# Kernel tuning notes

Hardware: AMD Instinct MI355X
Metric: run time of the kernel (lower is better)

The kernel has to match this reference:

```python
import jax, jax.numpy as jnp
import numpy as np

B, T, H, W, C = 8, 16, 128, 128, 3
PATCH = 8
MODEL_DIM = 512
FFN_DIM = 2048
NUM_BLOCKS = 4
NUM_HEADS = 8
LATENT_DIM = 64
NUM_LATENTS = 4096
ACTION_DIM = 16
PATCH_TOKEN_DIM = C * PATCH * PATCH  # 192


def setup_inputs() -> dict:
    key = jax.random.key(0)
    ks = jax.random.split(key, 12)
    g = lambda k, s: jax.random.normal(k, s, dtype=jnp.float32) * 0.02
    D, L = MODEL_DIM, NUM_BLOCKS
    return dict(
        videos=jax.random.uniform(ks[0], (B, T, H, W, C), dtype=jnp.float32),
        patch_w=g(ks[1], (PATCH_TOKEN_DIM, D)),
        patch_b=jnp.zeros((D,), jnp.float32),
        action_token=g(ks[2], (PATCH_TOKEN_DIM,)),
        ln1_g=jnp.ones((L, D), jnp.float32), ln1_b=jnp.zeros((L, D), jnp.float32),
        wqkv_s=g(ks[3], (L, D, 3 * D)), wo_s=g(ks[4], (L, D, D)),
        ln2_g=jnp.ones((L, D), jnp.float32), ln2_b=jnp.zeros((L, D), jnp.float32),
        wqkv_t=g(ks[5], (L, D, 3 * D)), wo_t=g(ks[6], (L, D, D)),
        ln3_g=jnp.ones((L, D), jnp.float32), ln3_b=jnp.zeros((L, D), jnp.float32),
        mlp_w1=g(ks[7], (L, D, FFN_DIM)), mlp_b1=jnp.zeros((L, FFN_DIM), jnp.float32),
        mlp_w2=g(ks[8], (L, FFN_DIM, D)), mlp_b2=jnp.zeros((L, D), jnp.float32),
        lnf_g=jnp.ones((D,), jnp.float32), lnf_b=jnp.zeros((D,), jnp.float32),
        out_w=g(ks[9], (D, LATENT_DIM)),
        codebook=g(ks[10], (NUM_LATENTS, LATENT_DIM)),
        action_w=g(ks[11], (LATENT_DIM, ACTION_DIM)),
    )


def _ln(x, g, b):
    m = jnp.mean(x, -1, keepdims=True)
    v = jnp.var(x, -1, keepdims=True)
    return (x - m) * jax.lax.rsqrt(v + 1e-5) * g + b


def _mha(x, wqkv, wo, causal):
    bsz, S, D = x.shape
    hd = D // NUM_HEADS
    q, k, v = jnp.split(x @ wqkv, 3, axis=-1)
    split = lambda t: t.reshape(bsz, S, NUM_HEADS, hd).transpose(0, 2, 1, 3)
    q, k, v = split(q), split(k), split(v)
    scores = jnp.einsum('bhqd,bhkd->bhqk', q, k) * (1.0 / np.sqrt(hd))
    if causal:
        mask = jnp.tril(jnp.ones((S, S), dtype=bool))
        scores = jnp.where(mask, scores, jnp.finfo(scores.dtype).min)
    o = jnp.einsum('bhqk,bhkd->bhqd', jax.nn.softmax(scores, axis=-1), v)
    return o.transpose(0, 2, 1, 3).reshape(bsz, S, D) @ wo


def _forward(videos, patch_w, patch_b, action_token, ln1_g, ln1_b, wqkv_s, wo_s,
             ln2_g, ln2_b, wqkv_t, wo_t, ln3_g, ln3_b, mlp_w1, mlp_b1, mlp_w2,
             mlp_b2, lnf_g, lnf_b, out_w, codebook, action_w):
    b, t = videos.shape[:2]
    hp, wp = H // PATCH, W // PATCH
    # patchify: (B,T,H,W,C) -> (B,T,N,p*p*C)
    x = videos.reshape(b, t, hp, PATCH, wp, PATCH, C)
    x = x.transpose(0, 1, 2, 4, 3, 5, 6).reshape(b, t, hp * wp, PATCH_TOKEN_DIM)
    # prepend learned action token per frame
    act = jnp.broadcast_to(action_token, (b, t, 1, PATCH_TOKEN_DIM))
    x = jnp.concatenate([act, x], axis=2)             # (B,T,S,Ep)
    S = x.shape[2]
    tok = x @ patch_w + patch_b                        # (B,T,S,D)
    for i in range(NUM_BLOCKS):
        # spatial attention within each frame
        h = _ln(tok, ln1_g[i], ln1_b[i]).reshape(b * t, S, MODEL_DIM)
        tok = tok + _mha(h, wqkv_s[i], wo_s[i], causal=False).reshape(b, t, S, MODEL_DIM)
        # temporal causal attention per spatial position
        h = _ln(tok, ln2_g[i], ln2_b[i]).transpose(0, 2, 1, 3).reshape(b * S, t, MODEL_DIM)
        h = _mha(h, wqkv_t[i], wo_t[i], causal=True)
        tok = tok + h.reshape(b, S, t, MODEL_DIM).transpose(0, 2, 1, 3)
        # MLP
        h = _ln(tok, ln3_g[i], ln3_b[i])
        tok = tok + jax.nn.gelu(h @ mlp_w1[i] + mlp_b1[i]) @ mlp_w2[i] + mlp_b2[i]
    tok = _ln(tok, lnf_g, lnf_b)
    # latent action per transition: action token of frames 1..T-1
    z = tok[:, 1:, 0, :] @ out_w                       # (B, T-1, latent_dim)
    # VQ: nearest-neighbor codebook lookup (squared-L2 argmin + gather)
    d = (jnp.sum(z * z, -1, keepdims=True)
         - 2.0 * (z @ codebook.T)
         + jnp.sum(codebook * codebook, -1))           # (B, T-1, num_latents)
    idx = jnp.argmin(d, axis=-1)                       # (B, T-1)
    z_q = codebook[idx]
    z_q = z + jax.lax.stop_gradient(z_q - z)           # straight-through
    latent_actions = jax.lax.stop_gradient(z_q)
    return latent_actions @ action_w                   # (B, T-1, action_dim)


def reference(videos, patch_w, patch_b, action_token, ln1_g, ln1_b, wqkv_s, wo_s,
              ln2_g, ln2_b, wqkv_t, wo_t, ln3_g, ln3_b, mlp_w1, mlp_b1, mlp_w2,
              mlp_b2, lnf_g, lnf_b, out_w, codebook, action_w):
    return _forward(videos, patch_w, patch_b, action_token, ln1_g, ln1_b, wqkv_s,
                    wo_s, ln2_g, ln2_b, wqkv_t, wo_t, ln3_g, ln3_b, mlp_w1,
                    mlp_b1, mlp_w2, mlp_b2, lnf_g, lnf_b, out_w, codebook, action_w)
```

## Files before the change

kernel.cpp:

```cpp
#include <hip/hip_runtime.h>
#include <hip/hip_bf16.h>

#define B_ 8
#define T_ 16
#define S_ 257
#define D_ 512
#define FFN_ 2048
#define NH_ 8
#define HD_ 64
#define PTD_ 192
#define NTOK (B_*T_*S_)
#define CH 4112
#define PCH 8224
#define WSCALE 64.0f
#define WINV 0.015625f

typedef unsigned int uint;
typedef unsigned short ushort;
typedef __attribute__((ext_vector_type(8))) _Float16 half8;
typedef __attribute__((ext_vector_type(4))) float f32x4;

__device__ __forceinline__ float warp_rsum(float v){
#pragma unroll
  for (int m = 32; m >= 1; m >>= 1) v += __shfl_xor(v, m);
  return v;
}
__device__ __forceinline__ float gelu_f(float x){
  float x3 = x*x*x;
  return 0.5f*x*(1.0f + tanhf(0.7978845608028654f*(x + 0.044715f*x3)));
}
__device__ __forceinline__ void split_f16(float f, ushort& h, ushort& l){
  _Float16 hh = (_Float16)f;
  float hf = (float)hh;
  _Float16 ll = (_Float16)(f - hf);
  h = __builtin_bit_cast(ushort, hh);
  l = __builtin_bit_cast(ushort, ll);
}
__device__ __forceinline__ ushort to_f16u(float f){
  return __builtin_bit_cast(ushort, (_Float16)f);
}
__device__ __forceinline__ float from_f16u(ushort u){
  return (float)__builtin_bit_cast(_Float16, u);
}
__device__ __forceinline__ void gload16(const ushort* g, ushort* l){
  __builtin_amdgcn_global_load_lds(
      (const __attribute__((address_space(1))) void*)(g),
      (__attribute__((address_space(3))) void*)(l),
      16, 0, 0);
}

__global__ __launch_bounds__(256) void ln_single(
    const float* __restrict__ x, const float* __restrict__ g,
    const float* __restrict__ bb, ushort* __restrict__ aH)
{
  int row = blockIdx.x * 4 + (threadIdx.x >> 6);
  int lane = threadIdx.x & 63;
  const float* xr = x + (long)row * D_;
  float4 u0 = *(const float4*)(xr + lane * 8);
  float4 u1 = *(const float4*)(xr + lane * 8 + 4);
  float s = u0.x + u0.y + u0.z + u0.w + u1.x + u1.y + u1.z + u1.w;
  s = warp_rsum(s);
  float mean = s * (1.0f / 512.0f);
  float d[8] = {u0.x - mean, u0.y - mean, u0.z - mean, u0.w - mean,
                u1.x - mean, u1.y - mean, u1.z - mean, u1.w - mean};
  float ss = 0.f;
#pragma unroll
  for (int i = 0; i < 8; i++) ss = fmaf(d[i], d[i], ss);
  ss = warp_rsum(ss);
  float rstd = rsqrtf(ss * (1.0f / 512.0f) + 1e-5f);
  int c = lane * 8;
  float4 g0 = *(const float4*)(g + c), g1 = *(const float4*)(g + c + 4);
  float4 b0 = *(const float4*)(bb + c), b1 = *(const float4*)(bb + c + 4);
  float y[8] = {d[0]*rstd*g0.x + b0.x, d[1]*rstd*g0.y + b0.y,
                d[2]*rstd*g0.z + b0.z, d[3]*rstd*g0.w + b0.w,
                d[4]*rstd*g1.x + b1.x, d[5]*rstd*g1.y + b1.y,
                d[6]*rstd*g1.z + b1.z, d[7]*rstd*g1.w + b1.w};
  ushort h[8];
#pragma unroll
  for (int i = 0; i < 8; i++) h[i] = to_f16u(y[i]);
  uint4 hv = make_uint4((uint)h[0] | ((uint)h[1] << 16), (uint)h[2] | ((uint)h[3] << 16),
                        (uint)h[4] | ((uint)h[5] << 16), (uint)h[6] | ((uint)h[7] << 16));
  *(uint4*)(aH + (long)row * 512 + c) = hv;
}

__global__ __launch_bounds__(256) void convert_w(
    const float* __restrict__ W, ushort* __restrict__ Whi, ushort* __restrict__ Wlo,
    int N, int K)
{
  __shared__ float Tt[64][65];
  const int tid = threadIdx.x;
  const int k0 = blockIdx.x << 6, n0 = blockIdx.y << 6;
  {
    int kk = tid >> 2, nb = (tid & 3) << 4;
#pragma unroll
    for (int q = 0; q < 4; q++) {
      float4 v = *(const float4*)(W + (long)(k0 + kk) * N + n0 + nb + 4 * q);
      Tt[kk][nb + 4*q + 0] = v.x; Tt[kk][nb + 4*q + 1] = v.y;
      Tt[kk][nb + 4*q + 2] = v.z; Tt[kk][nb + 4*q + 3] = v.w;
    }
  }
  __syncthreads();
  {
    int nn = tid >> 2, kb = (tid & 3) << 4;
    uint hw[8], lw[8];
#pragma unroll
    for (int q = 0; q < 8; q++) {
      float a = Tt[kb + 2*q][nn] * WSCALE, b = Tt[kb + 2*q + 1][nn] * WSCALE;
      ushort ha, la, hb, lb;
      split_f16(a, ha, la); split_f16(b, hb, lb);
      hw[q] = (uint)ha | ((uint)hb << 16); lw[q] = (uint)la | ((uint)lb << 16);
    }
    ushort* dh = Whi + (long)(n0 + nn) * K + k0 + kb;
    ushort* dl = Wlo + (long)(n0 + nn) * K + k0 + kb;
    ((uint4*)dh)[0] = make_uint4(hw[0], hw[1], hw[2], hw[3]);
    ((uint4*)dh)[1] = make_uint4(hw[4], hw[5], hw[6], hw[7]);
    ((uint4*)dl)[0] = make_uint4(lw[0], lw[1], lw[2], lw[3]);
    ((uint4*)dl)[1] = make_uint4(lw[4], lw[5], lw[6], lw[7]);
  }
}

template<int BM, int BN, int TM, int TN, int AMODE, bool ASPLIT, bool BSPLIT, bool BIAS, bool GELU, bool RESID, int SOUT>
__global__ __launch_bounds__(256) void gemm_mfma(
    const ushort* __restrict__ aHp, const ushort* __restrict__ aLp, int lda,
    const ushort* __restrict__ wtH, const ushort* __restrict__ wtL, int ldb,
    const float* __restrict__ bias, float* __restrict__ C,
    ushort* __restrict__ coH, ushort* __restrict__ vOut,
    const float* __restrict__ videos, const float* __restrict__ atok,
    int M, int N, int K)
{
  constexpr int NWC = BN / (TN * 16);
  constexpr int NBUF = (AMODE == 0) ? 2 : 1;
  __shared__ __align__(16) ushort sAh[NBUF * BM * 32];
  __shared__ __align__(16) ushort sAl[(AMODE == 1) ? 128 * 32 : 8];
  __shared__ __align__(16) ushort sBh[NBUF * BN * 32];
  __shared__ __align__(16) ushort sBl[BSPLIT ? NBUF * BN * 32 : 8];
  const int tid = threadIdx.x;
  int m0, n0;
  if (AMODE == 0) {
    const int gx = gridDim.x, gy = gridDim.y;
    const int nwg = gx * gy;
    const int o = blockIdx.y * gx + blockIdx.x;
    const int q = nwg >> 3, r = nwg & 7;
    const int xcd = o & 7, idx = o >> 3;
    const int wgid = (xcd < r ? xcd * (q + 1) : r * (q + 1) + (xcd - r) * q) + idx;
    const int mi = wgid / gy, ni = wgid - mi * gy;
    m0 = mi * BM; n0 = ni * BN;
  } else {
    m0 = blockIdx.x * BM; n0 = blockIdx.y * BN;
  }
  const int wid = tid >> 6, lane = tid & 63;
  const int lrow = lane & 15, lkg = lane >> 4;
  const int wr = wid / NWC, wc = wid % NWC;
  const int wrb = wr * TM * 16, wcb = wc * TN * 16;
  f32x4 acc[TM][TN];
#pragma unroll
  for (int mi = 0; mi < TM; mi++)
#pragma unroll
    for (int ni = 0; ni < TN; ni++) acc[mi][ni] = (f32x4){0.f, 0.f, 0.f, 0.f};

  if (AMODE == 0) {
    auto stage = [&](int k0, int d) {
      {
        int row = tid >> 2, cp = tid & 3;
        int csrc = cp ^ ((row >> 1) & 3);
        int ar = m0 + row; if (ar > M - 1) ar = M - 1;
        gload16(aHp + (long)ar * lda + k0 + csrc * 8, &sAh[d * (BM * 32) + tid * 8]);
      }
      if constexpr (BM == 128) {
        int chunk = tid + 256;
        int row = chunk >> 2, cp = chunk & 3;
        int csrc = cp ^ ((row >> 1) & 3);
        int ar = m0 + row; if (ar > M - 1) ar = M - 1;
        gload16(aHp + (long)ar * lda + k0 + csrc * 8, &sAh[d * (BM * 32) + chunk * 8]);
      }
      if (BN == 128) {
#pragma unroll
        for (int i = 0; i < 2; i++) {
          int chunk = tid + 256 * i;
          int row = chunk >> 2, cp = chunk & 3;
          int csrc = cp ^ ((row >> 1) & 3);
          gload16(wtH + (long)(n0 + row) * ldb + k0 + csrc * 8, &sBh[d * 4096 + chunk * 8]);
        }
      } else {
        int chunk = tid;
        int row = chunk >> 2, cp = chunk & 3;
        int csrc = cp ^ ((row >> 1) & 3);
        gload16(wtH + (long)(n0 + row) * ldb + k0 + csrc * 8, &sBh[d * 2048 + chunk * 8]);
        if (BSPLIT)
          gload16(wtL + (long)(n0 + row) * ldb + k0 + csrc * 8, &sBl[d * 2048 + chunk * 8]);
      }
    };
    const int nt = K >> 5;
    stage(0, 0);
    if (nt > 1) stage(32, 1);
    constexpr int LPS = ((BM == 128) ? 2 : 1) + ((BN == 128) ? 2 : (BSPLIT ? 2 : 1));
    for (int t = 0; t < nt; t++) {
      const int cur = t & 1;
      if (t + 1 < nt) {
        if constexpr (LPS == 4) {
          asm volatile("s_waitcnt vmcnt(4)" ::: "memory");
        } else if constexpr (LPS == 3) {
          asm volatile("s_waitcnt vmcnt(3)" ::: "memory");
        } else {
          asm volatile("s_waitcnt vmcnt(2)" ::: "memory");
        }
      } else {
        asm volatile("s_waitcnt vmcnt(0)" ::: "memory");
      }
      __builtin_amdgcn_s_barrier();
      const int aBase = cur * (BM * 32);
      const int bBase = cur * ((BN == 128) ? 4096 : 2048);
      half8 aHf[TM], bHf[TN], bLf[BSPLIT ? TN : 1];
#pragma unroll
      for (int mi = 0; mi < TM; mi++) {
        int ar = wrb + mi * 16 + lrow;
        int ac = (ar * 4 + (lkg ^ ((ar >> 1) & 3))) * 8;
        aHf[mi] = *(const half8*)&sAh[aBase + ac];
      }
#pragma unroll
      for (int ni = 0; ni < TN; ni++) {
        int br = wcb + ni * 16 + lrow;
        int bc = (br * 4 + (lkg ^ ((br >> 1) & 3))) * 8;
        bHf[ni] = *(const half8*)&sBh[bBase + bc];
        if (BSPLIT) bLf[ni] = *(const half8*)&sBl[bBase + bc];
      }
      asm volatile("s_waitcnt lgkmcnt(0)" ::: "memory");
      __builtin_amdgcn_sched_barrier(0);
      __builtin_amdgcn_s_barrier();
      if (t + 2 < nt) stage((t + 2) << 5, cur);
      __builtin_amdgcn_s_setprio(1);
#pragma unroll
      for (int ni = 0; ni < TN; ni++) {
        if (BSPLIT) {
#pragma unroll
          for (int mi = 0; mi < TM; mi++)
            acc[mi][ni] = __builtin_amdgcn_mfma_f32_16x16x32_f16(aHf[mi], bLf[ni], acc[mi][ni], 0, 0, 0);
        }
#pragma unroll
        for (int mi = 0; mi < TM; mi++)
          acc[mi][ni] = __builtin_amdgcn_mfma_f32_16x16x32_f16(aHf[mi], bHf[ni], acc[mi][ni], 0, 0, 0);
      }
      __builtin_amdgcn_s_setprio(0);
      __builtin_amdgcn_sched_barrier(0);
    }
  } else {
    const int rowa = tid >> 1, kba = (tid & 1) << 4;
    const int cb0 = (tid & 1) * 2;
    const int swa = (rowa >> 1) & 3;
    int bt_p = 0, s_p = 0;
    { int ar = m0 + rowa; bt_p = ar / 257; s_p = ar - bt_p * 257; }
    for (int k0 = 0; k0 < K; k0 += 32) {
      float4 vr[4];
#pragma unroll
      for (int q = 0; q < 4; q++) vr[q] = make_float4(0.f, 0.f, 0.f, 0.f);
#pragma unroll
      for (int q = 0; q < 4; q++) {
        int e4 = k0 + kba + 4 * q;
        if (s_p == 0) {
          vr[q] = *(const float4*)(atok + e4);
        } else {
          int p = s_p - 1, ph = p >> 4, pw = p & 15;
          int iq = e4 / 24, jc = e4 - iq * 24;
          vr[q] = *(const float4*)(videos + (long)bt_p * 49152 +
                                   (long)(ph * 8 + iq) * 384 + pw * 24 + jc);
        }
      }
      uint hw[8], lw[8];
#pragma unroll
      for (int q = 0; q < 4; q++) {
        ushort h0,l0,h1,l1,h2,l2,h3,l3;
        split_f16(vr[q].x, h0, l0); split_f16(vr[q].y, h1, l1);
        split_f16(vr[q].z, h2, l2); split_f16(vr[q].w, h3, l3);
        hw[2*q]   = (uint)h0 | ((uint)h1 << 16); lw[2*q]   = (uint)l0 | ((uint)l1 << 16);
        hw[2*q+1] = (uint)h2 | ((uint)h3 << 16); lw[2*q+1] = (uint)l2 | ((uint)l3 << 16);
      }
      *(uint4*)&sAh[(rowa * 4 + (cb0 ^ swa)) * 8]       = make_uint4(hw[0], hw[1], hw[2], hw[3]);
      *(uint4*)&sAh[(rowa * 4 + ((cb0 + 1) ^ swa)) * 8] = make_uint4(hw[4], hw[5], hw[6], hw[7]);
      *(uint4*)&sAl[(rowa * 4 + (cb0 ^ swa)) * 8]       = make_uint4(lw[0], lw[1], lw[2], lw[3]);
      *(uint4*)&sAl[(rowa * 4 + ((cb0 + 1) ^ swa)) * 8] = make_uint4(lw[4], lw[5], lw[6], lw[7]);
      {
#pragma unroll
        for (int i = 0; i < 2; i++) {
          int chunk = tid + 256 * i;
          int row = chunk >> 2, cp = chunk & 3;
          int csrc = cp ^ ((row >> 1) & 3);
          gload16(wtH + (long)(n0 + row) * ldb + k0 + csrc * 8, &sBh[chunk * 8]);
          if (BSPLIT)
            gload16(wtL + (long)(n0 + row) * ldb + k0 + csrc * 8, &sBl[chunk * 8]);
        }
      }
      __syncthreads();
      half8 aHf[TM], aLf[TM];
#pragma unroll
      for (int mi = 0; mi < TM; mi++) {
        int ar = wrb + mi * 16 + lrow;
        int ac = (ar * 4 + (lkg ^ ((ar >> 1) & 3))) * 8;
        aHf[mi] = *(const half8*)&sAh[ac];
        if (ASPLIT) aLf[mi] = *(const half8*)&sAl[ac];
      }
#pragma unroll
      for (int ni = 0; ni < TN; ni++) {
        int br = wcb + ni * 16 + lrow;
        int bc = (br * 4 + (lkg ^ ((br >> 1) & 3))) * 8;
        half8 bH = *(const half8*)&sBh[bc];
#pragma unroll
        for (int mi = 0; mi < TM; mi++) {
          if (ASPLIT)
            acc[mi][ni] = __builtin_amdgcn_mfma_f32_16x16x32_f16(aLf[mi], bH, acc[mi][ni], 0, 0, 0);
        }
        if (BSPLIT) {
          half8 bL = *(const half8*)&sBl[bc];
#pragma unroll
          for (int mi = 0; mi < TM; mi++)
            acc[mi][ni] = __builtin_amdgcn_mfma_f32_16x16x32_f16(aHf[mi], bL, acc[mi][ni], 0, 0, 0);
        }
#pragma unroll
        for (int mi = 0; mi < TM; mi++)
          acc[mi][ni] = __builtin_amdgcn_mfma_f32_16x16x32_f16(aHf[mi], bH, acc[mi][ni], 0, 0, 0);
      }
      __syncthreads();
    }
  }
#pragma unroll
  for (int mi = 0; mi < TM; mi++) {
    int rowg = m0 + wrb + mi * 16 + lkg * 4;
#pragma unroll
    for (int j = 0; j < 4; j++) {
      int r = rowg + j;
      if (r < M) {
#pragma unroll
        for (int ni = 0; ni < TN; ni++) {
          int cg = n0 + wcb + ni * 16 + lrow;
          float v = acc[mi][ni][j] * WINV;
          if (BIAS) v += bias[cg];
          if (GELU) v = gelu_f(v);
          if (SOUT == 2) {
            coH[(long)r * N + cg] = to_f16u(v);
          } else if (SOUT == 3) {
            if (cg < 1024) coH[(long)r * 1024 + cg] = to_f16u(v);
            else           vOut[(long)r * 512 + (cg - 1024)] = to_f16u(v);
          } else {
            long idx = (long)r * N + cg;
            if (RESID) C[idx] += v; else C[idx] = v;
          }
        }
      }
    }
  }
}

__global__ __launch_bounds__(256) void flash_spatial(
    const ushort* __restrict__ qk, const ushort* __restrict__ v2,
    ushort* __restrict__ ctxc)
{
  __shared__ __align__(16) ushort sQ[64*72];
  __shared__ __align__(16) ushort sK[64*72];
  __shared__ __align__(16) ushort sV[64*72];
  __shared__ __align__(16) ushort sP[64*72];
  const int tid = threadIdx.x;
  const int wid = tid >> 6, lane = tid & 63;
  const int lr = lane & 15, lg = lane >> 4;
  const int fh = blockIdx.y;
  const int fl = fh >> 3, hh = fh & 7;
  const int q0 = blockIdx.x * 64;
  const long rbase = (long)fl * S_;
  const int srow = tid >> 2, sc0 = (tid & 3) << 4;

  {
    int gr = q0 + srow;
    uint4 h0 = make_uint4(0,0,0,0), h1 = h0;
    if (gr < S_) {
      const ushort* sh = qk + (rbase + gr) * 1024 + hh * HD_ + sc0;
      h0 = ((const uint4*)sh)[0]; h1 = ((const uint4*)sh)[1];
    }
    uint4* dh = (uint4*)&sQ[srow*72 + sc0];
    dh[0] = h0; dh[1] = h1;
  }
  __syncthreads();
  half8 qH[2];
  {
    int qrl = wid * 16 + lr;
#pragma unroll
    for (int s = 0; s < 2; s++)
      qH[s] = *(const half8*)&sQ[qrl*72 + s*32 + lg*8];
  }
  f32x4 accS[5][4];
#pragma unroll
  for (int t = 0; t < 5; t++)
#pragma unroll
    for (int kc = 0; kc < 4; kc++) accS[t][kc] = (f32x4){0.f,0.f,0.f,0.f};

#pragma unroll
  for (int t = 0; t < 5; t++) {
    __syncthreads();
    {
      int gr = t*64 + srow;
      uint4 h0 = make_uint4(0,0,0,0), h1 = h0;
      if (gr < S_) {
        const ushort* sh = qk + (rbase + gr) * 1024 + 512 + hh * HD_ + sc0;
        h0 = ((const uint4*)sh)[0]; h1 = ((const uint4*)sh)[1];
      }
      uint4* dh = (uint4*)&sK[srow*72 + sc0];
      dh[0] = h0; dh[1] = h1;
    }
    __syncthreads();
#pragma unroll
    for (int s = 0; s < 2; s++) {
#pragma unroll
      for (int kc = 0; kc < 4; kc++) {
        int off = (kc*16 + lr)*72 + s*32 + lg*8;
        half8 bH = *(const half8*)&sK[off];
        accS[t][kc] = __builtin_amdgcn_mfma_f32_16x16x32_f16(qH[s], bH, accS[t][kc], 0,0,0);
      }
    }
  }

  float m[4] = {-3.0e38f, -3.0e38f, -3.0e38f, -3.0e38f};
#pragma unroll
  for (int t = 0; t < 5; t++)
#pragma unroll
    for (int kc = 0; kc < 4; kc++) {
      int kcol = t*64 + kc*16 + lr;
      if (kcol < S_) {
#pragma unroll
        for (int j = 0; j < 4; j++) m[j] = fmaxf(m[j], accS[t][kc][j] * 0.125f);
      }
    }
#pragma unroll
  for (int mk = 8; mk >= 1; mk >>= 1)
#pragma unroll
    for (int j = 0; j < 4; j++) m[j] = fmaxf(m[j], __shfl_xor(m[j], mk));
  float l[4] = {0.f, 0.f, 0.f, 0.f};
#pragma unroll
  for (int t = 0; t < 5; t++)
#pragma unroll
    for (int kc = 0; kc < 4; kc++) {
      int kcol = t*64 + kc*16 + lr;
#pragma unroll
      for (int j = 0; j < 4; j++) {
        float p = (kcol < S_) ? expf(accS[t][kc][j]*0.125f - m[j]) : 0.f;
        accS[t][kc][j] = p;
        l[j] += p;
      }
    }
#pragma unroll
  for (int mk = 8; mk >= 1; mk >>= 1)
#pragma unroll
    for (int j = 0; j < 4; j++) l[j] += __shfl_xor(l[j], mk);

  f32x4 accO[4];
#pragma unroll
  for (int dc = 0; dc < 4; dc++) accO[dc] = (f32x4){0.f,0.f,0.f,0.f};
#pragma unroll
  for (int t = 0; t < 5; t++) {
#pragma unroll
    for (int kc = 0; kc < 4; kc++)
#pragma unroll
      for (int j = 0; j < 4; j++) {
        int addr = (wid*16 + lg*4 + j)*72 + kc*16 + lr;
        sP[addr] = to_f16u(accS[t][kc][j]);
      }
    __syncthreads();
    {
      int gr = t*64 + srow;
      ushort tmp[16];
      uint4 a = make_uint4(0,0,0,0), b = a;
      if (gr < S_) {
        const ushort* src = v2 + (rbase + gr) * 512 + hh * HD_ + sc0;
        a = ((const uint4*)src)[0]; b = ((const uint4*)src)[1];
      }
      *(uint4*)&tmp[0] = a; *(uint4*)&tmp[8] = b;
#pragma unroll
      for (int e = 0; e < 16; e++) sV[(sc0 + e)*72 + srow] = tmp[e];
    }
    __syncthreads();
#pragma unroll
    for (int s = 0; s < 2; s++) {
      int poff = (wid*16 + lr)*72 + s*32 + lg*8;
      half8 pH = *(const half8*)&sP[poff];
#pragma unroll
      for (int dc = 0; dc < 4; dc++) {
        int voff = (dc*16 + lr)*72 + s*32 + lg*8;
        half8 vH = *(const half8*)&sV[voff];
        accO[dc] = __builtin_amdgcn_mfma_f32_16x16x32_f16(pH, vH, accO[dc], 0,0,0);
      }
    }
  }
#pragma unroll
  for (int j = 0; j < 4; j++) {
    int grow = q0 + wid*16 + lg*4 + j;
    if (grow < S_) {
      float inv = 1.0f / l[j];
#pragma unroll
      for (int dc = 0; dc < 4; dc++) {
        float o = accO[dc][j] * inv;
        long idx = (rbase + grow) * 512 + hh*64 + dc*16 + lr;
        ctxc[idx] = to_f16u(o);
      }
    }
  }
}

__global__ __launch_bounds__(64) void temporal_attn(
    const ushort* __restrict__ qk, const ushort* __restrict__ v2,
    ushort* __restrict__ ctxc)
{
  const int gid = blockIdx.x;
  const int b2 = gid / (S_ * NH_);
  const int rem = gid - b2 * S_ * NH_;
  const int hh = rem & 7;
  const int s = rem >> 3;
  const int lane = threadIdx.x;
  __shared__ float Qs[16][65];
  __shared__ float Ks[16][65];
  __shared__ float Pm[16][17];
  float v[16];
  const long rbase = (long)b2 * CH + s;
#pragma unroll
  for (int t = 0; t < 16; t++) {
    long row = rbase + (long)t * S_;
    long qoff = row * 1024 + hh * HD_ + lane;
    Qs[t][lane] = from_f16u(qk[qoff]);
    Ks[t][lane] = from_f16u(qk[qoff + 512]);
    v[t] = from_f16u(v2[row * 512 + hh * HD_ + lane]);
  }
  __syncthreads();
  const int rq = lane >> 2, c0 = lane & 3;
  float sc[4];
#pragma unroll
  for (int j = 0; j < 4; j++) {
    int c = c0 + (j << 2);
    if (c <= rq) {
      float d = 0.f;
#pragma unroll
      for (int k = 0; k < 64; k++) d = fmaf(Qs[rq][k], Ks[c][k], d);
      sc[j] = d * 0.125f;
    } else sc[j] = -3.0e38f;
  }
  float mx = fmaxf(fmaxf(sc[0], sc[1]), fmaxf(sc[2], sc[3]));
  mx = fmaxf(mx, __shfl_xor(mx, 1));
  mx = fmaxf(mx, __shfl_xor(mx, 2));
  float sum = 0.f;
#pragma unroll
  for (int j = 0; j < 4; j++) { sc[j] = expf(sc[j] - mx); sum += sc[j]; }
  sum += __shfl_xor(sum, 1);
  sum += __shfl_xor(sum, 2);
  float inv = 1.0f / sum;
#pragma unroll
  for (int j = 0; j < 4; j++) Pm[rq][c0 + (j << 2)] = sc[j] * inv;
  __syncthreads();
#pragma unroll
  for (int t = 0; t < 16; t++) {
    float o = 0.f;
#pragma unroll
    for (int k = 0; k < 16; k++) o = fmaf(Pm[t][k], v[k], o);
    long idx = (rbase + (long)t * S_) * 512 + hh * HD_ + lane;
    ctxc[idx] = to_f16u(o);
  }
}

__global__ __launch_bounds__(256) void final_vq(
    const float* __restrict__ tok, const float* __restrict__ lnf_g,
    const float* __restrict__ lnf_b, const float* __restrict__ out_w,
    const float* __restrict__ codebook, const float* __restrict__ action_w,
    float* __restrict__ out)
{
  __shared__ float xs[512];
  __shared__ float red[256];
  __shared__ float zs[64];
  __shared__ float bd[256];
  __shared__ int   bi[256];
  const int b = blockIdx.x / 15, tm = blockIdx.x % 15;
  const int tid = threadIdx.x;
  const float* xr = tok + ((long)(b * T_ + tm + 1) * S_) * D_;
  xs[tid] = xr[tid]; xs[tid + 256] = xr[tid + 256];
  red[tid] = xs[tid] + xs[tid + 256];
  __syncthreads();
  for (int off = 128; off >= 1; off >>= 1) {
    if (tid < off) red[tid] += red[tid + off];
    __syncthreads();
  }
  float mean = red[0] * (1.0f / 512.0f);
  __syncthreads();
  float d0 = xs[tid] - mean, d1 = xs[tid + 256] - mean;
  red[tid] = d0 * d0 + d1 * d1;
  __syncthreads();
  for (int off = 128; off >= 1; off >>= 1) {
    if (tid < off) red[tid] += red[tid + off];
    __syncthreads();
  }
  float rs = rsqrtf(red[0] * (1.0f / 512.0f) + 1e-5f);
  __syncthreads();
  xs[tid]       = d0 * rs * lnf_g[tid]       + lnf_b[tid];
  xs[tid + 256] = d1 * rs * lnf_g[tid + 256] + lnf_b[tid + 256];
  __syncthreads();
  if (tid < 64) {
    float z = 0.f;
    for (int d = 0; d < 512; d++) z = fmaf(xs[d], out_w[d * 64 + tid], z);
    zs[tid] = z;
  }
  __syncthreads();
  float best = 3.0e38f; int bidx = 0;
  for (int c = tid; c < 4096; c += 256) {
    const float* cp = codebook + (long)c * 64;
    float dot = 0.f, cn = 0.f;
#pragma unroll 8
    for (int k = 0; k < 64; k++) { float w = cp[k]; dot = fmaf(zs[k], w, dot); cn = fmaf(w, w, cn); }
    float dist = cn - 2.0f * dot;
    if (dist < best) { best = dist; bidx = c; }
  }
  bd[tid] = best; bi[tid] = bidx;
  __syncthreads();
  for (int off = 128; off >= 1; off >>= 1) {
    if (tid < off) {
      if (bd[tid + off] < bd[tid] || (bd[tid + off] == bd[tid] && bi[tid + off] < bi[tid])) {
        bd[tid] = bd[tid + off]; bi[tid] = bi[tid + off];
      }
    }
    __syncthreads();
  }
  int idx = bi[0];
  if (tid < 16) {
    const float* cp = codebook + (long)idx * 64;
    float o = 0.f;
#pragma unroll
    for (int k = 0; k < 64; k++) o = fmaf(cp[k], action_w[k * 16 + tid], o);
    out[((long)(b * 15 + tm)) * 16 + tid] = o;
  }
}

extern "C" void kernel_launch(void* const* d_in, const int* in_sizes, int n_in,
                              void* d_out, int out_size, void* d_ws, size_t ws_size,
                              hipStream_t stream)
{
  const float* videos       = (const float*)d_in[0];
  const float* patch_w      = (const float*)d_in[1];
  const float* patch_b      = (const float*)d_in[2];
  const float* action_token = (const float*)d_in[3];
  const float* ln1_g  = (const float*)d_in[4];
  const float* ln1_b  = (const float*)d_in[5];
  const float* wqkv_s = (const float*)d_in[6];
  const float* wo_s   = (const float*)d_in[7];
  const float* ln2_g  = (const float*)d_in[8];
  const float* ln2_b  = (const float*)d_in[9];
  const float* wqkv_t = (const float*)d_in[10];
  const float* wo_t   = (const float*)d_in[11];
  const float* ln3_g  = (const float*)d_in[12];
  const float* ln3_b  = (const float*)d_in[13];
  const float* mlp_w1 = (const float*)d_in[14];
  const float* mlp_b1 = (const float*)d_in[15];
  const float* mlp_w2 = (const float*)d_in[16];
  const float* mlp_b2 = (const float*)d_in[17];
  const float* lnf_g  = (const float*)d_in[18];
  const float* lnf_b  = (const float*)d_in[19];
  const float* out_w  = (const float*)d_in[20];
  const float* codebook = (const float*)d_in[21];
  const float* action_w = (const float*)d_in[22];
  float* out = (float*)d_out;

  float* ws    = (float*)d_ws;
  float* tok   = ws;
  ushort* wt1h = (ushort*)(ws + 16842752);
  ushort* wt1l = wt1h + 1048576;
  ushort* wt2h = (ushort*)(ws + 17891328);
  ushort* wt2l = wt2h + 1048576;
  ushort* aH   = (ushort*)(ws + 18939904);
  ushort* qk   = (ushort*)(ws + 21045248);
  ushort* v2   = (ushort*)(ws + 25255936);
  ushort* ctx  = (ushort*)(ws + 27361280);
  ushort* mid  = qk;

  convert_w<<<dim3(3, 8), 256, 0, stream>>>(patch_w, wt1h, wt1l, 512, 192);
  gemm_mfma<128,128,4,4,1,true,true,true,false,false,0><<<dim3(257, 4), 256, 0, stream>>>(
      nullptr, nullptr, 0, wt1h, wt1l, 192, patch_b, tok, nullptr, nullptr,
      videos, action_token, NTOK, 512, 192);

  for (int L = 0; L < 4; L++) {
    convert_w<<<dim3(8, 24), 256, 0, stream>>>(wqkv_s + (long)L*512*1536, wt1h, wt1l, 1536, 512);
    convert_w<<<dim3(8, 8),  256, 0, stream>>>(wo_s   + (long)L*512*512,  wt2h, wt2l, 512, 512);
    for (int pr = 0; pr < 4; pr++) {
      long r0 = (long)pr * PCH;
      ln_single<<<PCH / 4, 256, 0, stream>>>(tok + r0 * D_, ln1_g + L*512, ln1_b + L*512, aH);
      gemm_mfma<64,128,2,4,0,false,false,false,false,false,3><<<dim3(129, 12), 256, 0, stream>>>(
          aH, nullptr, 512, wt1h, wt1l, 512, nullptr, nullptr,
          qk, v2, nullptr, nullptr, PCH, 1536, 512);
      flash_spatial<<<dim3(5, 256), 256, 0, stream>>>(qk, v2, ctx);
      gemm_mfma<128,64,2,4,0,false,false,false,false,true,0><<<dim3(65, 8), 256, 0, stream>>>(
          ctx, nullptr, 512, wt2h, wt2l, 512, nullptr, tok + r0 * D_,
          nullptr, nullptr, nullptr, nullptr, PCH, 512, 512);
    }
    convert_w<<<dim3(8, 24), 256, 0, stream>>>(wqkv_t + (long)L*512*1536, wt1h, wt1l, 1536, 512);
    convert_w<<<dim3(8, 8),  256, 0, stream>>>(wo_t   + (long)L*512*512,  wt2h, wt2l, 512, 512);
    for (int pr = 0; pr < 4; pr++) {
      long r0 = (long)pr * PCH;
      ln_single<<<PCH / 4, 256, 0, stream>>>(tok + r0 * D_, ln2_g + L*512, ln2_b + L*512, aH);
      gemm_mfma<64,128,2,4,0,false,false,false,false,false,3><<<dim3(129, 12), 256, 0, stream>>>(
          aH, nullptr, 512, wt1h, wt1l, 512, nullptr, nullptr,
          qk, v2, nullptr, nullptr, PCH, 1536, 512);
      temporal_attn<<<2 * S_ * NH_, 64, 0, stream>>>(qk, v2, ctx);
      gemm_mfma<128,64,2,4,0,false,false,false,false,true,0><<<dim3(65, 8), 256, 0, stream>>>(
          ctx, nullptr, 512, wt2h, wt2l, 512, nullptr, tok + r0 * D_,
          nullptr, nullptr, nullptr, nullptr, PCH, 512, 512);
    }
    convert_w<<<dim3(8, 32), 256, 0, stream>>>(mlp_w1 + (long)L*512*2048, wt1h, wt1l, 2048, 512);
    convert_w<<<dim3(32, 8), 256, 0, stream>>>(mlp_w2 + (long)L*2048*512, wt2h, wt2l, 512, 2048);
    for (int c = 0; c < 4; c++) {
      long m0r = (long)c * PCH;
      ln_single<<<PCH / 4, 256, 0, stream>>>(tok + m0r * D_, ln3_g + L*512, ln3_b + L*512, aH);
      gemm_mfma<64,128,2,4,0,false,false,true,true,false,2><<<dim3(129, 16), 256, 0, stream>>>(
          aH, nullptr, 512, wt1h, wt1l, 512, mlp_b1 + (long)L*2048, nullptr, mid, nullptr,
          nullptr, nullptr, PCH, FFN_, 512);
      gemm_mfma<128,64,2,4,0,false,false,true,false,true,0><<<dim3(65, 8), 256, 0, stream>>>(
          mid, nullptr, 2048, wt2h, wt2l, 2048, mlp_b2 + (long)L*512, tok + m0r * D_,
          nullptr, nullptr, nullptr, nullptr, PCH, 512, 2048);
    }
  }

  final_vq<<<B_ * (T_ - 1), 256, 0, stream>>>(tok, lnf_g, lnf_b, out_w, codebook, action_w, out);
}
```

Measured before the change: 3.866 ms.

## Shrink N=512 GEMM tiles for more blocks and parallelize final VQ kernel

The output-projection and MLP-down GEMMs (N=512) switch from 128x64 tiles to 64x64 tiles, doubling the grid from 65x8 to 129x8 blocks so more of the GPU's compute units are busy. The final VQ kernel now runs 1024 threads per block. It uses wave-shuffle reductions for the layernorm and argmin, splits the out_w projection across all threads, and reads the codebook with float4 loads. Smaller tiles lower per-block data reuse and add more B-operand traffic. The VQ kernel is a tiny fraction of total time.

```diff
diff --git a/kernel.cpp b/kernel.cpp
--- a/kernel.cpp
+++ b/kernel.cpp
@@ -559,67 +559,90 @@
   }
 }
 
-__global__ __launch_bounds__(256) void final_vq(
+__global__ __launch_bounds__(1024) void final_vq(
     const float* __restrict__ tok, const float* __restrict__ lnf_g,
     const float* __restrict__ lnf_b, const float* __restrict__ out_w,
     const float* __restrict__ codebook, const float* __restrict__ action_w,
     float* __restrict__ out)
 {
   __shared__ float xs[512];
-  __shared__ float red[256];
+  __shared__ float red[16];
+  __shared__ float zp[1024];
   __shared__ float zs[64];
-  __shared__ float bd[256];
-  __shared__ int   bi[256];
+  __shared__ float bd[16];
+  __shared__ int   bi[16];
+  __shared__ int   bsel;
   const int b = blockIdx.x / 15, tm = blockIdx.x % 15;
   const int tid = threadIdx.x;
+  const int wv = tid >> 6, lane = tid & 63;
   const float* xr = tok + ((long)(b * T_ + tm + 1) * S_) * D_;
-  xs[tid] = xr[tid]; xs[tid + 256] = xr[tid + 256];
-  red[tid] = xs[tid] + xs[tid + 256];
-  __syncthreads();
-  for (int off = 128; off >= 1; off >>= 1) {
-    if (tid < off) red[tid] += red[tid + off];
-    __syncthreads();
-  }
-  float mean = red[0] * (1.0f / 512.0f);
-  __syncthreads();
-  float d0 = xs[tid] - mean, d1 = xs[tid + 256] - mean;
-  red[tid] = d0 * d0 + d1 * d1;
-  __syncthreads();
-  for (int off = 128; off >= 1; off >>= 1) {
-    if (tid < off) red[tid] += red[tid + off];
-    __syncthreads();
-  }
-  float rs = rsqrtf(red[0] * (1.0f / 512.0f) + 1e-5f);
-  __syncthreads();
-  xs[tid]       = d0 * rs * lnf_g[tid]       + lnf_b[tid];
-  xs[tid + 256] = d1 * rs * lnf_g[tid + 256] + lnf_b[tid + 256];
+  float x0 = (tid < 512) ? xr[tid] : 0.f;
+  float s = warp_rsum(x0);
+  if (lane == 0) red[wv] = s;
+  __syncthreads();
+  float tot = 0.f;
+#pragma unroll
+  for (int w = 0; w < 16; w++) tot += red[w];
+  float mean = tot * (1.0f / 512.0f);
+  float dv = (tid < 512) ? (x0 - mean) : 0.f;
+  __syncthreads();
+  float ss = warp_rsum(dv * dv);
+  if (lane == 0) red[wv] = ss;
+  __syncthreads();
+  float vtot = 0.f;
+#pragma unroll
+  for (int w = 0; w < 16; w++) vtot += red[w];
+  float rstd = rsqrtf(vtot * (1.0f / 512.0f) + 1e-5f);
+  if (tid < 512) xs[tid] = dv * rstd * lnf_g[tid] + lnf_b[tid];
+  __syncthreads();
+  {
+    int o = tid & 63, p = tid >> 6;
+    int d0 = p * 32;
+    float z = 0.f;
+#pragma unroll 8
+    for (int k = 0; k < 32; k++) z = fmaf(xs[d0 + k], out_w[(long)(d0 + k) * 64 + o], z);
+    zp[tid] = z;
+  }
   __syncthreads();
   if (tid < 64) {
     float z = 0.f;
-    for (int d = 0; d < 512; d++) z = fmaf(xs[d], out_w[d * 64 + tid], z);
+#pragma unroll
+    for (int p = 0; p < 16; p++) z += zp[p * 64 + tid];
     zs[tid] = z;
   }
   __syncthreads();
   float best = 3.0e38f; int bidx = 0;
-  for (int c = tid; c < 4096; c += 256) {
-    const float* cp = codebook + (long)c * 64;
+  for (int c = tid; c < 4096; c += 1024) {
+    const float4* cp = (const float4*)(codebook + (long)c * 64);
     float dot = 0.f, cn = 0.f;
-#pragma unroll 8
-    for (int k = 0; k < 64; k++) { float w = cp[k]; dot = fmaf(zs[k], w, dot); cn = fmaf(w, w, cn); }
+#pragma unroll
+    for (int k = 0; k < 16; k++) {
+      float4 w = cp[k];
+      dot = fmaf(zs[4*k + 0], w.x, dot); cn = fmaf(w.x, w.x, cn);
+      dot = fmaf(zs[4*k + 1], w.y, dot); cn = fmaf(w.y, w.y, cn);
+      dot = fmaf(zs[4*k + 2], w.z, dot); cn = fmaf(w.z, w.z, cn);
+      dot = fmaf(zs[4*k + 3], w.w, dot); cn = fmaf(w.w, w.w, cn);
+    }
     float dist = cn - 2.0f * dot;
     if (dist < best) { best = dist; bidx = c; }
   }
-  bd[tid] = best; bi[tid] = bidx;
-  __syncthreads();
-  for (int off = 128; off >= 1; off >>= 1) {
-    if (tid < off) {
-      if (bd[tid + off] < bd[tid] || (bd[tid + off] == bd[tid] && bi[tid + off] < bi[tid])) {
-        bd[tid] = bd[tid + off]; bi[tid] = bi[tid + off];
-      }
-    }
-    __syncthreads();
-  }
-  int idx = bi[0];
+#pragma unroll
+  for (int mk = 32; mk >= 1; mk >>= 1) {
+    float ob = __shfl_xor(best, mk);
+    int   oi = __shfl_xor(bidx, mk);
+    if (ob < best || (ob == best && oi < bidx)) { best = ob; bidx = oi; }
+  }
+  if (lane == 0) { bd[wv] = best; bi[wv] = bidx; }
+  __syncthreads();
+  if (tid == 0) {
+    float bb = bd[0]; int ii = bi[0];
+#pragma unroll
+    for (int w = 1; w < 16; w++)
+      if (bd[w] < bb || (bd[w] == bb && bi[w] < ii)) { bb = bd[w]; ii = bi[w]; }
+    bsel = ii;
+  }
+  __syncthreads();
+  int idx = bsel;
   if (tid < 16) {
     const float* cp = codebook + (long)idx * 64;
     float o = 0.f;
@@ -685,7 +708,7 @@
           aH, nullptr, 512, wt1h, wt1l, 512, nullptr, nullptr,
           qk, v2, nullptr, nullptr, PCH, 1536, 512);
       flash_spatial<<<dim3(5, 256), 256, 0, stream>>>(qk, v2, ctx);
-      gemm_mfma<128,64,2,4,0,false,false,false,false,true,0><<<dim3(65, 8), 256, 0, stream>>>(
+      gemm_mfma<64,64,1,4,0,false,false,false,false,true,0><<<dim3(129, 8), 256, 0, stream>>>(
           ctx, nullptr, 512, wt2h, wt2l, 512, nullptr, tok + r0 * D_,
           nullptr, nullptr, nullptr, nullptr, PCH, 512, 512);
     }
@@ -698,7 +721,7 @@
           aH, nullptr, 512, wt1h, wt1l, 512, nullptr, nullptr,
           qk, v2, nullptr, nullptr, PCH, 1536, 512);
       temporal_attn<<<2 * S_ * NH_, 64, 0, stream>>>(qk, v2, ctx);
-      gemm_mfma<128,64,2,4,0,false,false,false,false,true,0><<<dim3(65, 8), 256, 0, stream>>>(
+      gemm_mfma<64,64,1,4,0,false,false,false,false,true,0><<<dim3(129, 8), 256, 0, stream>>>(
           ctx, nullptr, 512, wt2h, wt2l, 512, nullptr, tok + r0 * D_,
           nullptr, nullptr, nullptr, nullptr, PCH, 512, 512);
     }
@@ -710,11 +733,11 @@
       gemm_mfma<64,128,2,4,0,false,false,true,true,false,2><<<dim3(129, 16), 256, 0, stream>>>(
           aH, nullptr, 512, wt1h, wt1l, 512, mlp_b1 + (long)L*2048, nullptr, mid, nullptr,
           nullptr, nullptr, PCH, FFN_, 512);
-      gemm_mfma<128,64,2,4,0,false,false,true,false,true,0><<<dim3(65, 8), 256, 0, stream>>>(
+      gemm_mfma<64,64,1,4,0,false,false,true,false,true,0><<<dim3(129, 8), 256, 0, stream>>>(
           mid, nullptr, 2048, wt2h, wt2l, 2048, mlp_b2 + (long)L*512, tok + m0r * D_,
           nullptr, nullptr, nullptr, nullptr, PCH, 512, 2048);
     }
   }
 
-  final_vq<<<B_ * (T_ - 1), 256, 0, stream>>>(tok, lnf_g, lnf_b, out_w, codebook, action_w, out);
-}
+  final_vq<<<B_ * (T_ - 1), 1024, 0, stream>>>(tok, lnf_g, lnf_b, out_w, codebook, action_w, out);
+}
```

Measured after the change: 3.832 ms. About the same (-0.9%).
